# Kernel optimization log

Measured on AMD Instinct MI355X. Metric: run time of the kernel, lower is better.

The kernel has to match this reference:

```python
import jax, jax.numpy as jnp
import numpy as np

N_NODES = 100000
N_EDGES = 3200000
N_RELS = 8
F_IN = 64
F_OUT = 64


def setup_inputs() -> dict:
    key = jax.random.key(0)
    k1, k2, k3, k4, k5, k6 = jax.random.split(key, 6)
    X = jax.random.normal(k1, (N_NODES, F_IN), dtype=jnp.float32)
    W = jax.random.normal(k2, (N_RELS, F_IN, F_OUT), dtype=jnp.float32) * 0.1
    A = jax.random.uniform(k3, (N_EDGES,), dtype=jnp.float32)
    src = jax.random.randint(k4, (N_EDGES,), 0, N_NODES, dtype=jnp.int32)
    dst = jax.random.randint(k5, (N_EDGES,), 0, N_NODES, dtype=jnp.int32)
    etype = jax.random.randint(k6, (N_EDGES,), 0, N_RELS, dtype=jnp.int32)
    return {"X": X, "W": W, "A": A, "src": src, "dst": dst, "etype": etype}


def reference(X, W, A, src, dst, etype):
    # RGCN hetero forward: Y[i,fo] = sum_{r,j in N_r(i)} A[r,i,j] * (X[j] @ W[r])[fo]
    # Precompute per-relation transformed features: [R, N, F_out]
    XW = jnp.einsum('nf,rfo->rno', X, W)
    # Gather per-edge message and scale by edge weight: [E, F_out]
    msg = XW[etype, src] * A[:, None]
    # Scatter-add into destination nodes: [N, F_out]
    Y = jax.ops.segment_sum(msg, dst, num_segments=X.shape[0])
    return Y
```

## Files before the change

kernel.cpp:

```cpp
#include <hip/hip_runtime.h>
#include <hip/hip_fp16.h>

#define FDIM 64
#define P_BLK 1024
#define NSB_MAX 32
#define SB_BITS 12
#define SB_PAD 135168
#define CHUNK_CAP 3200
#define CHUNK2 4224
#define SPB 32
#define NB_MAX 800
#define BKT_NODES 128
#define SEG_PAD 4608
#define SEG_CAP 4608
#define OVF_CAP 64
#define CUR_STRIDE 16
#define FUSED_LDS 46080

typedef __attribute__((ext_vector_type(8))) short short8;
typedef __attribute__((ext_vector_type(4))) float float4_;

__device__ __forceinline__ unsigned short f2bf(float x) {
    unsigned u = __float_as_uint(x);
    return (unsigned short)((u + 0x7FFF + ((u >> 16) & 1)) >> 16);
}

__global__ __launch_bounds__(1024) void init_cursors(
    int* __restrict__ gcur1, int* __restrict__ gcur2, int NSB, int B)
{
    const int t = (int)(blockIdx.x * 1024 + threadIdx.x);
    if (t < NSB) gcur1[t * CUR_STRIDE] = t * SB_PAD;
    if (t < B)   gcur2[t * CUR_STRIDE] = t * SEG_PAD;
}

__global__ __launch_bounds__(256) void gemm_coarse_fused(
    const float* __restrict__ X, const float* __restrict__ Wmat,
    __half* __restrict__ XWh,
    const int* __restrict__ src, const int* __restrict__ dst,
    const int* __restrict__ etype, const float* __restrict__ A,
    int* __restrict__ gcur1, int2* __restrict__ packed1,
    int E, int N, int R, int NSB, int chunk, int gemmBlocks, int totalBlocks)
{
    extern __shared__ char smem[];
    const int bid = (int)blockIdx.x;
    const int tid = threadIdx.x;
    const int gcount = (int)(((long)bid * gemmBlocks) / totalBlocks);
    const int gnext  = (int)(((long)(bid + 1) * gemmBlocks) / totalBlocks);

    if (gnext > gcount) {
        unsigned short* Wt = (unsigned short*)smem;
        unsigned short* Ot = Wt + 4 * 64 * 72;
        const int gb_id = gcount;
        const int rp    = gb_id & 1;
        const int blockBase = (gb_id >> 1) * 256;
        const int lane = tid & 63;
        const int wave = tid >> 6;
        const int quad = lane >> 4;
        const int l15  = lane & 15;
        unsigned short* Otw = Ot + wave * 16 * 72;

        short8 bfrag[4][2];
        bool tvalid[4];
#pragma unroll
        for (int t = 0; t < 4; ++t) {
            const int tb = blockBase + (wave * 4 + t) * 16;
            tvalid[t] = (tb < N);
            if (tvalid[t]) {
                const float* xp = X + (size_t)(tb + l15) * FDIM + quad * 8;
                const float4 x0 = *(const float4*)(xp);
                const float4 x1 = *(const float4*)(xp + 4);
                const float4 x2 = *(const float4*)(xp + 32);
                const float4 x3 = *(const float4*)(xp + 36);
                short8 b0, b1;
                b0[0]=f2bf(x0.x); b0[1]=f2bf(x0.y); b0[2]=f2bf(x0.z); b0[3]=f2bf(x0.w);
                b0[4]=f2bf(x1.x); b0[5]=f2bf(x1.y); b0[6]=f2bf(x1.z); b0[7]=f2bf(x1.w);
                b1[0]=f2bf(x2.x); b1[1]=f2bf(x2.y); b1[2]=f2bf(x2.z); b1[3]=f2bf(x2.w);
                b1[4]=f2bf(x3.x); b1[5]=f2bf(x3.y); b1[6]=f2bf(x3.z); b1[7]=f2bf(x3.w);
                bfrag[t][0] = b0; bfrag[t][1] = b1;
            } else {
                bfrag[t][0] = (short8)(0); bfrag[t][1] = (short8)(0);
            }
        }

#pragma unroll
        for (int it = 0; it < 16; ++it) {
            const int idx = it * 256 + tid;
            const int k  = idx & 63;
            const int f4 = (idx >> 6) & 15;
            const int r  = idx >> 10;
            const float4 w = *(const float4*)(Wmat + (((size_t)(rp * 4 + r) * FDIM + k) * FDIM + f4 * 4));
            const int base = (r * 64 + f4 * 4) * 72 + k;
            Wt[base + 0 * 72] = f2bf(w.x);
            Wt[base + 1 * 72] = f2bf(w.y);
            Wt[base + 2 * 72] = f2bf(w.z);
            Wt[base + 3 * 72] = f2bf(w.w);
        }
        __syncthreads();

#pragma unroll
        for (int t = 0; t < 4; ++t) {
            if (!tvalid[t]) continue;
            const int tb = blockBase + (wave * 4 + t) * 16;
#pragma unroll
            for (int r = 0; r < 4; ++r) {
#pragma unroll
                for (int ft = 0; ft < 4; ++ft) {
                    const int f = ft * 16 + l15;
                    const unsigned short* wp = &Wt[(r * 64 + f) * 72 + quad * 8];
                    const short8 a0 = *(const short8*)(wp);
                    const short8 a1 = *(const short8*)(wp + 32);
                    float4_ acc = {0.f, 0.f, 0.f, 0.f};
                    acc = __builtin_amdgcn_mfma_f32_16x16x32_bf16(a0, bfrag[t][0], acc, 0, 0, 0);
                    acc = __builtin_amdgcn_mfma_f32_16x16x32_bf16(a1, bfrag[t][1], acc, 0, 0, 0);
                    const __half2 h01 = __floats2half2_rn(acc[0], acc[1]);
                    const __half2 h23 = __floats2half2_rn(acc[2], acc[3]);
                    uint2 st;
                    st.x = *(const unsigned*)&h01;
                    st.y = *(const unsigned*)&h23;
                    *(uint2*)&Otw[l15 * 72 + ft * 16 + quad * 4] = st;
                }
                const int node = lane >> 2;
                const int c    = lane & 3;
                const uint4 w0 = *(const uint4*)&Otw[node * 72 + c * 16];
                const uint4 w1 = *(const uint4*)&Otw[node * 72 + c * 16 + 8];
                __half* orow = XWh + ((size_t)(rp * 4 + r) * N + (tb + node)) * FDIM;
                *(uint4*)(orow + c * 16)     = w0;
                *(uint4*)(orow + c * 16 + 8) = w1;
            }
        }
    } else {
        int* lcnt = (int*)smem;
        int* gb   = lcnt + NSB_MAX;
        int2* recs = (int2*)(smem + 256);
        unsigned char* rbkt = (unsigned char*)(recs + CHUNK_CAP);
        const int p = bid - gcount;
        const int i0 = p * chunk, iend = min(i0 + chunk, E);

        if (tid < NSB_MAX) lcnt[tid] = 0;
        __syncthreads();
        for (int i = i0 + tid; i < iend; i += 256)
            atomicAdd(&lcnt[dst[i] >> SB_BITS], 1);
        __syncthreads();

        if (tid < 64) {
            const int c = (tid < NSB) ? lcnt[tid] : 0;
            int v = c;
#pragma unroll
            for (int o = 1; o < 64; o <<= 1) {
                const int u = __shfl_up(v, o, 64);
                if (tid >= o) v += u;
            }
            if (tid < NSB) gb[tid] = v - c;
        }
        __syncthreads();
        if (tid < NSB) {
            const int c = lcnt[tid];
            const int pfx = gb[tid];
            const int rbase = c ? atomicAdd(&gcur1[tid * CUR_STRIDE], c) : 0;
            gb[tid] = rbase - pfx;
            lcnt[tid] = pfx;
        }
        __syncthreads();

        for (int i = i0 + tid; i < iend; i += 256) {
            const int d = dst[i];
            const int sb = d >> SB_BITS;
            const int slot = atomicAdd(&lcnt[sb], 1);
            recs[slot] = make_int2((etype[i] * N + src[i]) | ((d & 127) << 20) | (((d >> 7) & 31) << 27),
                                   __float_as_int(A[i]));
            rbkt[slot] = (unsigned char)sb;
        }
        __syncthreads();

        const int tot = iend - i0;
        for (int s = tid; s < tot; s += 256) {
            const int b = rbkt[s];
            const int gi = gb[b] + s;
            if (gi < (b + 1) * SB_PAD)
                packed1[gi] = recs[s];
        }
    }
}

__global__ __launch_bounds__(256) void scatter_fine(
    const int2* __restrict__ packed1, const int* __restrict__ gcur1,
    int* __restrict__ gcur2, int2* __restrict__ packed2, int B)
{
    __shared__ int lcnt[32];
    __shared__ int gb[32];
    __shared__ int2 recs[CHUNK2];
    __shared__ unsigned char rbkt[CHUNK2];
    const int sb  = (int)blockIdx.x >> 5;
    const int cix = (int)blockIdx.x & 31;
    const int tid = threadIdx.x;
    const int sbBase = sb * SB_PAD;
    const int sbCnt = min(gcur1[sb * CUR_STRIDE] - sbBase, SB_PAD);
    const int i0 = cix * CHUNK2, iend = min(i0 + CHUNK2, sbCnt);
    if (i0 >= sbCnt) return;

    if (tid < 32) lcnt[tid] = 0;
    __syncthreads();
    for (int i = i0 + tid; i < iend; i += 256)
        atomicAdd(&lcnt[(packed1[sbBase + i].x >> 27) & 31], 1);
    __syncthreads();

    if (tid < 64) {
        const int c = (tid < 32) ? lcnt[tid] : 0;
        int v = c;
#pragma unroll
        for (int o = 1; o < 64; o <<= 1) {
            const int u = __shfl_up(v, o, 64);
            if (tid >= o) v += u;
        }
        if (tid < 32) gb[tid] = v - c;
    }
    __syncthreads();
    if (tid < 32) {
        const int bglob = sb * 32 + tid;
        const int c = lcnt[tid];
        const int pfx = gb[tid];
        const int rbase = (c && bglob < B) ? atomicAdd(&gcur2[bglob * CUR_STRIDE], c) : 0;
        gb[tid] = rbase - pfx;
        lcnt[tid] = pfx;
    }
    __syncthreads();

    for (int i = i0 + tid; i < iend; i += 256) {
        const int2 rec = packed1[sbBase + i];
        const int fb = (rec.x >> 27) & 31;
        const int slot = atomicAdd(&lcnt[fb], 1);
        recs[slot] = rec;
        rbkt[slot] = (unsigned char)fb;
    }
    __syncthreads();

    const int tot = iend - i0;
    for (int s = tid; s < tot; s += 256) {
        const int fb = rbkt[s];
        const int gi = gb[fb] + s;
        if (gi < (sb * 32 + fb + 1) * SEG_PAD)
            packed2[gi] = recs[s];
    }
}

__global__ __launch_bounds__(512) void agg_fused(
    const __half* __restrict__ XWh, const int2* __restrict__ packed,
    const int* __restrict__ gcur, float* __restrict__ Y, int N)
{
    __shared__ int2 recs[SEG_CAP];
    __shared__ int hist[BKT_NODES];
    __shared__ int pfx[BKT_NODES + 1];
    __shared__ int cur[BKT_NODES];
    __shared__ int2 ovf[OVF_CAP];
    __shared__ int ovfN;
    const int bkt = blockIdx.x, tid = threadIdx.x;
    const int segBase = bkt * SEG_PAD;
    const int cnt = min(gcur[bkt * CUR_STRIDE] - segBase, SEG_PAD);

    if (tid < BKT_NODES) hist[tid] = 0;
    if (tid == 0) ovfN = 0;
    __syncthreads();
    for (int i = tid; i < cnt; i += 512)
        atomicAdd(&hist[(packed[segBase + i].x >> 20) & 127], 1);
    __syncthreads();
    if (tid < 64) {
        int carry = 0;
#pragma unroll
        for (int t0 = 0; t0 < BKT_NODES; t0 += 64) {
            const int b = t0 + tid;
            const int c = hist[b];
            int v = c;
#pragma unroll
            for (int o = 1; o < 64; o <<= 1) {
                const int u = __shfl_up(v, o, 64);
                if (tid >= o) v += u;
            }
            pfx[b] = carry + v - c;
            cur[b] = carry + v - c;
            carry += __shfl(v, 63, 64);
            if (tid == 0 && t0 + 64 == BKT_NODES) pfx[BKT_NODES] = carry;
        }
    }
    __syncthreads();
    for (int i = tid; i < cnt; i += 512) {
        const int2 rec = packed[segBase + i];
        const int dl = (rec.x >> 20) & 127;
        const int pos = atomicAdd(&cur[dl], 1);
        if (pos < SEG_CAP) recs[pos] = rec;
        else { const int o = atomicAdd(&ovfN, 1); if (o < OVF_CAP) ovf[o] = rec; }
    }
    __syncthreads();

    const int lane = tid & 63;
    const int w    = tid >> 6;
    const int el   = lane >> 4;
    const int fl4  = lane & 15;
    const __half2* __restrict__ XW2 = (const __half2*)XWh;
    const unsigned foff = (unsigned)(fl4 << 1);

    for (int j = 0; j < 16; ++j) {
        const int nl = w * 16 + j;
        const int gnode = bkt * BKT_NODES + nl;
        if (gnode >= N) break;
        const int beg = min(pfx[nl], SEG_CAP);
        const int end = min(pfx[nl + 1], SEG_CAP);
        float4_ acc = {0.f, 0.f, 0.f, 0.f};
        for (int b2 = beg; b2 < end; b2 += 64) {
            const int idx = b2 + lane;
            const int2 ka = (idx < end) ? recs[idx] : make_int2(0, 0);
            const int nb = min(64, end - b2);
            const int nsteps = (((nb + 3) >> 2) + 7) & ~7;
            for (int s = 0; s < nsteps; s += 8) {
                int k[8], bv[8];
#pragma unroll
                for (int u = 0; u < 8; ++u) {
                    const int jj = ((s + u) << 2) + el;
                    k[u]  = __shfl(ka.x, jj, 64);
                    bv[u] = __shfl(ka.y, jj, 64);
                }
                uint2 v[8];
#pragma unroll
                for (int u = 0; u < 8; ++u)
                    v[u] = *(const uint2*)(XW2 + ((((unsigned)k[u]) & 0xFFFFFu) << 5) + foff);
#pragma unroll
                for (int u = 0; u < 8; ++u) {
                    const float a = __int_as_float(bv[u]);
                    const float2 f0 = __half22float2(*(const __half2*)&v[u].x);
                    const float2 f1 = __half22float2(*(const __half2*)&v[u].y);
                    acc[0] += a * f0.x; acc[1] += a * f0.y;
                    acc[2] += a * f1.x; acc[3] += a * f1.y;
                }
            }
        }
#pragma unroll
        for (int m = 16; m <= 32; m <<= 1) {
            acc[0] += __shfl_xor(acc[0], m, 64);
            acc[1] += __shfl_xor(acc[1], m, 64);
            acc[2] += __shfl_xor(acc[2], m, 64);
            acc[3] += __shfl_xor(acc[3], m, 64);
        }
        if (lane < 16)
            *(float4_*)(Y + (size_t)gnode * FDIM + (fl4 << 2)) = acc;
    }
    __syncthreads();

    const int no = min(ovfN, OVF_CAP);
    for (int o = tid; o < no; o += 512) {
        const int2 rec = ovf[o];
        const int node = bkt * BKT_NODES + ((rec.x >> 20) & 127);
        if (node < N) {
            const float a = __int_as_float(rec.y);
            const __half* row = XWh + (size_t)(rec.x & 0xFFFFF) * FDIM;
            for (int f = 0; f < FDIM; ++f)
                atomicAdd(&Y[(size_t)node * FDIM + f], a * __half2float(row[f]));
        }
    }
}

extern "C" void kernel_launch(void* const* d_in, const int* in_sizes, int n_in,
                              void* d_out, int out_size, void* d_ws, size_t ws_size,
                              hipStream_t stream)
{
    const float* X     = (const float*)d_in[0];
    const float* Wmat  = (const float*)d_in[1];
    const float* A     = (const float*)d_in[2];
    const int*   src   = (const int*)d_in[3];
    const int*   dst   = (const int*)d_in[4];
    const int*   etype = (const int*)d_in[5];
    float* Y = (float*)d_out;

    const int N = in_sizes[0] / FDIM;
    const int R = in_sizes[1] / (FDIM * FDIM);
    const int E = in_sizes[2];
    (void)n_in; (void)out_size; (void)ws_size;

    const int B   = (N + BKT_NODES - 1) / BKT_NODES;
    const int NSB = (N + (1 << SB_BITS) - 1) >> SB_BITS;
    const int chunk = (E + P_BLK - 1) / P_BLK;
    const int gemmBlocks  = ((N + 255) / 256) * 2;
    const int totalBlocks = gemmBlocks + P_BLK;

    char* ws = (char*)d_ws;
    size_t off = 0;
    auto take = [&](size_t bytes) { char* p = ws + off; off = (off + bytes + 255) & ~(size_t)255; return p; };
    __half* XWh     = (__half*)take((size_t)R * N * FDIM * sizeof(__half));
    int2*   packed1 = (int2*)  take((size_t)NSB * SB_PAD * sizeof(int2));
    int2*   packed2 = (int2*)  take((size_t)B * SEG_PAD * sizeof(int2));
    int*    gcur1   = (int*)   take((size_t)NSB * CUR_STRIDE * sizeof(int));
    int*    gcur2   = (int*)   take((size_t)B * CUR_STRIDE * sizeof(int));

    init_cursors<<<1, 1024, 0, stream>>>(gcur1, gcur2, NSB, B);
    gemm_coarse_fused<<<totalBlocks, 256, FUSED_LDS, stream>>>(
        X, Wmat, XWh, src, dst, etype, A, gcur1, packed1,
        E, N, R, NSB, chunk, gemmBlocks, totalBlocks);
    scatter_fine<<<NSB * SPB, 256, 0, stream>>>(packed1, gcur1, gcur2, packed2, B);
    agg_fused<<<B, 512, 0, stream>>>(XWh, packed2, gcur2, Y, N);
}
```

Measured before the change: 287.4 us.

## Co-schedule GEMM with fine scatter instead of coarse scatter

Result: slower. 330.0 us (+14.8%).

```diff
diff --git a/kernel.cpp b/kernel.cpp
--- a/kernel.cpp
+++ b/kernel.cpp
@@ -15,7 +15,8 @@
 #define SEG_CAP 4608
 #define OVF_CAP 64
 #define CUR_STRIDE 16
-#define FUSED_LDS 46080
+#define WTS 70
+#define FUSED_LDS 45056
 
 typedef __attribute__((ext_vector_type(8))) short short8;
 typedef __attribute__((ext_vector_type(4))) float float4_;
@@ -33,13 +34,70 @@
     if (t < B)   gcur2[t * CUR_STRIDE] = t * SEG_PAD;
 }
 
-__global__ __launch_bounds__(256) void gemm_coarse_fused(
-    const float* __restrict__ X, const float* __restrict__ Wmat,
-    __half* __restrict__ XWh,
+__global__ __launch_bounds__(256) void scatter_coarse(
     const int* __restrict__ src, const int* __restrict__ dst,
     const int* __restrict__ etype, const float* __restrict__ A,
     int* __restrict__ gcur1, int2* __restrict__ packed1,
-    int E, int N, int R, int NSB, int chunk, int gemmBlocks, int totalBlocks)
+    int E, int N, int NSB, int chunk)
+{
+    __shared__ int lcnt[NSB_MAX];
+    __shared__ int gb[NSB_MAX];
+    __shared__ int2 recs[CHUNK_CAP];
+    __shared__ unsigned char rbkt[CHUNK_CAP];
+    const int p = blockIdx.x, tid = threadIdx.x;
+    const int i0 = p * chunk, iend = min(i0 + chunk, E);
+
+    if (tid < NSB_MAX) lcnt[tid] = 0;
+    __syncthreads();
+    for (int i = i0 + tid; i < iend; i += 256)
+        atomicAdd(&lcnt[dst[i] >> SB_BITS], 1);
+    __syncthreads();
+
+    if (tid < 64) {
+        const int c = (tid < NSB) ? lcnt[tid] : 0;
+        int v = c;
+#pragma unroll
+        for (int o = 1; o < 64; o <<= 1) {
+            const int u = __shfl_up(v, o, 64);
+            if (tid >= o) v += u;
+        }
+        if (tid < NSB) gb[tid] = v - c;
+    }
+    __syncthreads();
+    if (tid < NSB) {
+        const int c = lcnt[tid];
+        const int pfx = gb[tid];
+        const int rbase = c ? atomicAdd(&gcur1[tid * CUR_STRIDE], c) : 0;
+        gb[tid] = rbase - pfx;
+        lcnt[tid] = pfx;
+    }
+    __syncthreads();
+
+    for (int i = i0 + tid; i < iend; i += 256) {
+        const int d = dst[i];
+        const int sb = d >> SB_BITS;
+        const int slot = atomicAdd(&lcnt[sb], 1);
+        recs[slot] = make_int2((etype[i] * N + src[i]) | ((d & 127) << 20) | (((d >> 7) & 31) << 27),
+                               __float_as_int(A[i]));
+        rbkt[slot] = (unsigned char)sb;
+    }
+    __syncthreads();
+
+    const int tot = iend - i0;
+    for (int s = tid; s < tot; s += 256) {
+        const int b = rbkt[s];
+        const int gi = gb[b] + s;
+        if (gi < (b + 1) * SB_PAD)
+            packed1[gi] = recs[s];
+    }
+}
+
+__global__ __launch_bounds__(256) void gemm_fine_fused(
+    const float* __restrict__ X, const float* __restrict__ Wmat,
+    __half* __restrict__ XWh,
+    const int2* __restrict__ packed1, const int* __restrict__ gcur1,
+    int* __restrict__ gcur2, int2* __restrict__ packed2,
+    int N, int B, int gemmBlocks, int totalBlocks)
 {
     extern __shared__ char smem[];
     const int bid = (int)blockIdx.x;
@@ -49,7 +107,7 @@
 
     if (gnext > gcount) {
         unsigned short* Wt = (unsigned short*)smem;
-        unsigned short* Ot = Wt + 4 * 64 * 72;
+        unsigned short* Ot = Wt + 4 * 64 * WTS;
         const int gb_id = gcount;
         const int rp    = gb_id & 1;
         const int blockBase = (gb_id >> 1) * 256;
@@ -89,11 +147,11 @@
             const int f4 = (idx >> 6) & 15;
             const int r  = idx >> 10;
             const float4 w = *(const float4*)(Wmat + (((size_t)(rp * 4 + r) * FDIM + k) * FDIM + f4 * 4));
-            const int base = (r * 64 + f4 * 4) * 72 + k;
-            Wt[base + 0 * 72] = f2bf(w.x);
-            Wt[base + 1 * 72] = f2bf(w.y);
-            Wt[base + 2 * 72] = f2bf(w.z);
-            Wt[base + 3 * 72] = f2bf(w.w);
+            const int base = (r * 64 + f4 * 4) * WTS + k;
+            Wt[base + 0 * WTS] = f2bf(w.x);
+            Wt[base + 1 * WTS] = f2bf(w.y);
+            Wt[base + 2 * WTS] = f2bf(w.z);
+            Wt[base + 3 * WTS] = f2bf(w.w);
         }
         __syncthreads();
 
@@ -106,7 +164,7 @@
 #pragma unroll
                 for (int ft = 0; ft < 4; ++ft) {
                     const int f = ft * 16 + l15;
-                    const unsigned short* wp = &Wt[(r * 64 + f) * 72 + quad * 8];
+                    const unsigned short* wp = &Wt[(r * 64 + f) * WTS + quad * 8];
                     const short8 a0 = *(const short8*)(wp);
                     const short8 a1 = *(const short8*)(wp + 32);
                     float4_ acc = {0.f, 0.f, 0.f, 0.f};
@@ -130,116 +188,60 @@
         }
     } else {
         int* lcnt = (int*)smem;
-        int* gb   = lcnt + NSB_MAX;
+        int* gb   = lcnt + 32;
         int2* recs = (int2*)(smem + 256);
-        unsigned char* rbkt = (unsigned char*)(recs + CHUNK_CAP);
-        const int p = bid - gcount;
-        const int i0 = p * chunk, iend = min(i0 + chunk, E);
-
-        if (tid < NSB_MAX) lcnt[tid] = 0;
+        unsigned char* rbkt = (unsigned char*)(recs + CHUNK2);
+        const int p   = bid - gcount;
+        const int sb  = p >> 5;
+        const int cix = p & 31;
+        const int sbBase = sb * SB_PAD;
+        const int sbCnt = min(gcur1[sb * CUR_STRIDE] - sbBase, SB_PAD);
+        const int i0 = cix * CHUNK2, iend = min(i0 + CHUNK2, sbCnt);
+        if (i0 >= sbCnt) return;
+
+        if (tid < 32) lcnt[tid] = 0;
         __syncthreads();
         for (int i = i0 + tid; i < iend; i += 256)
-            atomicAdd(&lcnt[dst[i] >> SB_BITS], 1);
+            atomicAdd(&lcnt[(packed1[sbBase + i].x >> 27) & 31], 1);
         __syncthreads();
 
         if (tid < 64) {
-            const int c = (tid < NSB) ? lcnt[tid] : 0;
+            const int c = (tid < 32) ? lcnt[tid] : 0;
             int v = c;
 #pragma unroll
             for (int o = 1; o < 64; o <<= 1) {
                 const int u = __shfl_up(v, o, 64);
                 if (tid >= o) v += u;
             }
-            if (tid < NSB) gb[tid] = v - c;
-        }
-        __syncthreads();
-        if (tid < NSB) {
+            if (tid < 32) gb[tid] = v - c;
+        }
+        __syncthreads();
+        if (tid < 32) {
+            const int bglob = sb * 32 + tid;
             const int c = lcnt[tid];
             const int pfx = gb[tid];
-            const int rbase = c ? atomicAdd(&gcur1[tid * CUR_STRIDE], c) : 0;
+            const int rbase = (c && bglob < B) ? atomicAdd(&gcur2[bglob * CUR_STRIDE], c) : 0;
             gb[tid] = rbase - pfx;
             lcnt[tid] = pfx;
         }
         __syncthreads();
 
         for (int i = i0 + tid; i < iend; i += 256) {
-            const int d = dst[i];
-            const int sb = d >> SB_BITS;
-            const int slot = atomicAdd(&lcnt[sb], 1);
-            recs[slot] = make_int2((etype[i] * N + src[i]) | ((d & 127) << 20) | (((d >> 7) & 31) << 27),
-                                   __float_as_int(A[i]));
-            rbkt[slot] = (unsigned char)sb;
+            const int2 rec = packed1[sbBase + i];
+            const int fb = (rec.x >> 27) & 31;
+            const int slot = atomicAdd(&lcnt[fb], 1);
+            recs[slot] = rec;
+            rbkt[slot] = (unsigned char)fb;
         }
         __syncthreads();
 
         const int tot = iend - i0;
         for (int s = tid; s < tot; s += 256) {
-            const int b = rbkt[s];
-            const int gi = gb[b] + s;
-            if (gi < (b + 1) * SB_PAD)
-                packed1[gi] = recs[s];
-        }
-    }
-}
-
-__global__ __launch_bounds__(256) void scatter_fine(
-    const int2* __restrict__ packed1, const int* __restrict__ gcur1,
-    int* __restrict__ gcur2, int2* __restrict__ packed2, int B)
-{
-    __shared__ int lcnt[32];
-    __shared__ int gb[32];
-    __shared__ int2 recs[CHUNK2];
-    __shared__ unsigned char rbkt[CHUNK2];
-    const int sb  = (int)blockIdx.x >> 5;
-    const int cix = (int)blockIdx.x & 31;
-    const int tid = threadIdx.x;
-    const int sbBase = sb * SB_PAD;
-    const int sbCnt = min(gcur1[sb * CUR_STRIDE] - sbBase, SB_PAD);
-    const int i0 = cix * CHUNK2, iend = min(i0 + CHUNK2, sbCnt);
-    if (i0 >= sbCnt) return;
-
-    if (tid < 32) lcnt[tid] = 0;
-    __syncthreads();
-    for (int i = i0 + tid; i < iend; i += 256)
-        atomicAdd(&lcnt[(packed1[sbBase + i].x >> 27) & 31], 1);
-    __syncthreads();
-
-    if (tid < 64) {
-        const int c = (tid < 32) ? lcnt[tid] : 0;
-        int v = c;
-#pragma unroll
-        for (int o = 1; o < 64; o <<= 1) {
-            const int u = __shfl_up(v, o, 64);
-            if (tid >= o) v += u;
-        }
-        if (tid < 32) gb[tid] = v - c;
-    }
-    __syncthreads();
-    if (tid < 32) {
-        const int bglob = sb * 32 + tid;
-        const int c = lcnt[tid];
-        const int pfx = gb[tid];
-        const int rbase = (c && bglob < B) ? atomicAdd(&gcur2[bglob * CUR_STRIDE], c) : 0;
-        gb[tid] = rbase - pfx;
-        lcnt[tid] = pfx;
-    }
-    __syncthreads();
-
-    for (int i = i0 + tid; i < iend; i += 256) {
-        const int2 rec = packed1[sbBase + i];
-        const int fb = (rec.x >> 27) & 31;
-        const int slot = atomicAdd(&lcnt[fb], 1);
-        recs[slot] = rec;
-        rbkt[slot] = (unsigned char)fb;
-    }
-    __syncthreads();
-
-    const int tot = iend - i0;
-    for (int s = tid; s < tot; s += 256) {
-        const int fb = rbkt[s];
-        const int gi = gb[fb] + s;
-        if (gi < (sb * 32 + fb + 1) * SEG_PAD)
-            packed2[gi] = recs[s];
+            const int fb = rbkt[s];
+            const int gi = gb[fb] + s;
+            if (gi < (sb * 32 + fb + 1) * SEG_PAD)
+                packed2[gi] = recs[s];
+        }
     }
 }
 
@@ -372,13 +374,14 @@
     const int N = in_sizes[0] / FDIM;
     const int R = in_sizes[1] / (FDIM * FDIM);
     const int E = in_sizes[2];
-    (void)n_in; (void)out_size; (void)ws_size;
+    (void)n_in; (void)out_size; (void)ws_size; (void)R;
 
     const int B   = (N + BKT_NODES - 1) / BKT_NODES;
     const int NSB = (N + (1 << SB_BITS) - 1) >> SB_BITS;
     const int chunk = (E + P_BLK - 1) / P_BLK;
     const int gemmBlocks  = ((N + 255) / 256) * 2;
-    const int totalBlocks = gemmBlocks + P_BLK;
+    const int fineBlocks  = NSB * SPB;
+    const int totalBlocks = gemmBlocks + fineBlocks;
 
     char* ws = (char*)d_ws;
     size_t off = 0;
@@ -390,9 +393,8 @@
     int*    gcur2   = (int*)   take((size_t)B * CUR_STRIDE * sizeof(int));
 
     init_cursors<<<1, 1024, 0, stream>>>(gcur1, gcur2, NSB, B);
-    gemm_coarse_fused<<<totalBlocks, 256, FUSED_LDS, stream>>>(
-        X, Wmat, XWh, src, dst, etype, A, gcur1, packed1,
-        E, N, R, NSB, chunk, gemmBlocks, totalBlocks);
-    scatter_fine<<<NSB * SPB, 256, 0, stream>>>(packed1, gcur1, gcur2, packed2, B);
+    scatter_coarse<<<P_BLK, 256, 0, stream>>>(src, dst, etype, A, gcur1, packed1, E, N, NSB, chunk);
+    gemm_fine_fused<<<totalBlocks, 256, FUSED_LDS, stream>>>(
+        X, Wmat, XWh, packed1, gcur1, gcur2, packed2, N, B, gemmBlocks, totalBlocks);
     agg_fused<<<B, 512, 0, stream>>>(XWh, packed2, gcur2, Y, N);
 }
```
